# Kernel optimization log

Measured on AMD Instinct MI355X. Metric: run time of the kernel, lower is better.

## Reference

```python
import jax, jax.numpy as jnp
import numpy as np

N = 1024
BATCH = 256


def setup_inputs() -> dict:
    key = jax.random.key(0)
    k1, k2 = jax.random.split(key)
    log_alpha = jax.random.normal(k1, (BATCH, N), dtype=jnp.float32)
    W = jax.random.normal(k2, (N, N), dtype=jnp.float32)  # unnormalized transition matrix
    return {"log_alpha": log_alpha, "W": W}


def reference(log_alpha, W):
    # log_softmax over dim=0 (columns are distributions over next state)
    log_T = jax.nn.log_softmax(W, axis=0)  # [N, N]
    # log_domain_matmul: out[i, m] = logsumexp_j( log_T[i, j] + log_alpha[m, j] )
    # then transpose back -> out[m, i]
    # broadcast-add cube [BATCH, N, N] then logsumexp over j (tropical-semiring matmul)
    out = jax.scipy.special.logsumexp(
        log_T[None, :, :] + log_alpha[:, None, :], axis=2
    )  # [BATCH, N]
    return out
```

## Files before the change

### kernel.cpp

```cpp
#include <hip/hip_runtime.h>
#include <hip/hip_bf16.h>

#define N 1024
#define BATCH 256
#define LPAD 136

typedef __attribute__((ext_vector_type(4))) short short4v;
typedef __attribute__((ext_vector_type(8))) short short8;
typedef __attribute__((ext_vector_type(4))) float f32x4;

static __device__ __forceinline__ ushort bfbits(float f) {
    union { __hip_bfloat16 h; ushort u; } cv; cv.h = __float2bfloat16(f); return cv.u;
}
static __device__ __forceinline__ float bf2f(ushort u) {
    union { ushort u; __hip_bfloat16 h; } cv; cv.u = u; return __bfloat162float(cv.h);
}

__global__ __launch_bounds__(256) void k1_psplit(const float* __restrict__ W,
                                                 float* __restrict__ psum,
                                                 ushort* __restrict__ Ph,
                                                 ushort* __restrict__ Pl) {
    const int t = threadIdx.x, lane = t & 63, w = t >> 6;
    const int cg = blockIdx.x & 3, slab = blockIdx.x >> 2;
    const int c = cg * 256 + lane * 4;
    __shared__ f32x4 sm[4][64];
    f32x4 acc = {0.f, 0.f, 0.f, 0.f};
#pragma unroll
    for (int it = 0; it < 4; ++it) {
        const int row = slab * 16 + w * 4 + it;
        const f32x4 v = *(const f32x4*)(W + row * N + c);
        short4v ph, pl;
        f32x4 e;
#pragma unroll
        for (int x = 0; x < 4; ++x) {
            e[x] = __expf(v[x]);
            const ushort h = bfbits(e[x]);
            ph[x] = (short)h;
            pl[x] = (short)bfbits(e[x] - bf2f(h));
        }
        *(short4v*)(Ph + row * N + c) = ph;
        *(short4v*)(Pl + row * N + c) = pl;
        acc += e;
    }
    sm[w][lane] = acc;
    __syncthreads();
    if (t < 64)
        *(f32x4*)(psum + slab * N + c) =
            sm[0][lane] + sm[1][lane] + sm[2][lane] + sm[3][lane];
}

__global__ __launch_bounds__(256) void k2_qsplit(const float* __restrict__ la,
                                                 const float* __restrict__ psum,
                                                 ushort* __restrict__ Qh,
                                                 ushort* __restrict__ Ql) {
    const int t = threadIdx.x;
    const int cg = blockIdx.x & 7, mg = blockIdx.x >> 3;
    const int c0 = cg * 128;
    __shared__ f32x4 smred[8][32];
    __shared__ float lcs[128];

    const int q = t & 31, sg = t >> 5;
    f32x4 a = {0.f, 0.f, 0.f, 0.f};
#pragma unroll
    for (int i = 0; i < 8; ++i)
        a += *(const f32x4*)(psum + (sg * 8 + i) * N + c0 + q * 4);
    smred[sg][q] = a;
    __syncthreads();
    if (t < 32) {
        f32x4 s = {0.f, 0.f, 0.f, 0.f};
#pragma unroll
        for (int g = 0; g < 8; ++g) s += smred[g][t];
#pragma unroll
        for (int x = 0; x < 4; ++x) lcs[t * 4 + x] = __logf(s[x]);
    }
    __syncthreads();

    const int row = mg * 16 + (t >> 4);
    const int cc  = (t & 15) * 8;
    const float* pla = la + row * N + c0 + cc;
    const f32x4 v0 = *(const f32x4*)(pla);
    const f32x4 v1 = *(const f32x4*)(pla + 4);
    short8 qh, ql;
#pragma unroll
    for (int x = 0; x < 8; ++x) {
        const float lv = (x < 4) ? v0[x] : v1[x - 4];
        const float qv = __expf(lv - lcs[cc + x]);
        const ushort h = bfbits(qv);
        qh[x] = (short)h;
        ql[x] = (short)bfbits(qv - bf2f(h));
    }
    *(short8*)(Qh + row * N + c0 + cc) = qh;
    *(short8*)(Ql + row * N + c0 + cc) = ql;
}

__global__ __launch_bounds__(512) void k3_mm(const ushort* __restrict__ Qh,
                                             const ushort* __restrict__ Ql,
                                             const ushort* __restrict__ Ph,
                                             const ushort* __restrict__ Pl,
                                             float* __restrict__ out) {
    __shared__ ushort sQh[32 * LPAD], sQl[32 * LPAD];
    __shared__ ushort sPh[32 * LPAD], sPl[32 * LPAD];

    const int t    = threadIdx.x;
    const int lane = t & 63;
    const int wid  = t >> 6;
    const int wm   = (wid >> 1) & 1;
    const int wn   = wid & 1;
    const int g    = wid >> 2;
    const int m0   = (blockIdx.x >> 5) * 32;
    const int i0   = (blockIdx.x & 31) * 32;

    const int srow = t >> 4;
    const int skc  = (t & 15) * 8;
    const ushort* gQh = Qh + (m0 + srow) * N + skc;
    const ushort* gQl = Ql + (m0 + srow) * N + skc;
    const ushort* gPh = Ph + (i0 + srow) * N + skc;
    const ushort* gPl = Pl + (i0 + srow) * N + skc;
    const int sdst = srow * LPAD + skc;

    const int aoff = (wm * 16 + (lane & 15)) * LPAD + g * 64 + (lane >> 4) * 8;
    const int boff = (wn * 16 + (lane & 15)) * LPAD + g * 64 + (lane >> 4) * 8;

    f32x4 acc = {0.f, 0.f, 0.f, 0.f};

    short8 vqh = *(const short8*)(gQh);
    short8 vql = *(const short8*)(gQl);
    short8 vph = *(const short8*)(gPh);
    short8 vpl = *(const short8*)(gPl);

    for (int k0 = 0; k0 < N; k0 += 128) {
        __syncthreads();
        *(short8*)&sQh[sdst] = vqh;
        *(short8*)&sQl[sdst] = vql;
        *(short8*)&sPh[sdst] = vph;
        *(short8*)&sPl[sdst] = vpl;
        if (k0 + 128 < N) {
            vqh = *(const short8*)(gQh + k0 + 128);
            vql = *(const short8*)(gQl + k0 + 128);
            vph = *(const short8*)(gPh + k0 + 128);
            vpl = *(const short8*)(gPl + k0 + 128);
        }
        __syncthreads();
#pragma unroll
        for (int ks = 0; ks < 2; ++ks) {
            const short8 aQh = *(const short8*)&sQh[aoff + ks * 32];
            const short8 aQl = *(const short8*)&sQl[aoff + ks * 32];
            const short8 bPh = *(const short8*)&sPh[boff + ks * 32];
            const short8 bPl = *(const short8*)&sPl[boff + ks * 32];
            acc = __builtin_amdgcn_mfma_f32_16x16x32_bf16(aQh, bPh, acc, 0, 0, 0);
            acc = __builtin_amdgcn_mfma_f32_16x16x32_bf16(aQh, bPl, acc, 0, 0, 0);
            acc = __builtin_amdgcn_mfma_f32_16x16x32_bf16(aQl, bPh, acc, 0, 0, 0);
        }
    }

    __syncthreads();
    f32x4* red = (f32x4*)sQh;
    red[wid * 64 + lane] = acc;
    __syncthreads();
    if (wid < 4) {
        const f32x4 s = red[wid * 64 + lane] + red[(wid + 4) * 64 + lane];
        const int om = m0 + wm * 16 + (lane >> 4) * 4;
        const int oi = i0 + wn * 16 + (lane & 15);
#pragma unroll
        for (int r = 0; r < 4; ++r)
            out[(om + r) * N + oi] = __logf(s[r]);
    }
}

extern "C" void kernel_launch(void* const* d_in, const int* in_sizes, int n_in,
                              void* d_out, int out_size, void* d_ws, size_t ws_size,
                              hipStream_t stream) {
    const float* la = (const float*)d_in[0];
    const float* W  = (const float*)d_in[1];
    float* out = (float*)d_out;

    char* ws = (char*)d_ws;
    float*  psum = (float*)ws;
    ushort* Ph   = (ushort*)(ws + (256 << 10));
    ushort* Pl   = Ph + (size_t)N * N;
    ushort* Qh   = Pl + (size_t)N * N;
    ushort* Ql   = Qh + (size_t)BATCH * N;

    k1_psplit<<<256, 256, 0, stream>>>(W, psum, Ph, Pl);
    k2_qsplit<<<128, 256, 0, stream>>>(la, psum, Qh, Ql);
    k3_mm<<<256, 512, 0, stream>>>(Qh, Ql, Ph, Pl, out);
}
```

Before: 68.65 us.

## Load MFMA operands directly from global into registers, drop LDS staging

The matmul kernel no longer stages Q and P tiles through shared memory. Each wave loads its MFMA fragments straight from global memory into a register double buffer, prefetching the second half of its K range while computing the first, and splits the work across two accumulators to shorten the dependency chain. This removes the per-step LDS writes, reads and barriers, at the cost of more registers and global loads that are less coalesced. The Q-prep kernel is also regridded to twice as many blocks, each handling 64 columns, to spread that work across more CUs.

After: 78.50 us. 1.14x slower.

```diff
diff --git a/kernel.cpp b/kernel.cpp
--- a/kernel.cpp
+++ b/kernel.cpp
@@ -3,7 +3,6 @@
 
 #define N 1024
 #define BATCH 256
-#define LPAD 136
 
 typedef __attribute__((ext_vector_type(4))) short short4v;
 typedef __attribute__((ext_vector_type(8))) short short8;
@@ -54,43 +53,37 @@
                                                  ushort* __restrict__ Qh,
                                                  ushort* __restrict__ Ql) {
     const int t = threadIdx.x;
-    const int cg = blockIdx.x & 7, mg = blockIdx.x >> 3;
-    const int c0 = cg * 128;
-    __shared__ f32x4 smred[8][32];
-    __shared__ float lcs[128];
+    const int cg = blockIdx.x & 15, mg = blockIdx.x >> 4;
+    const int c0 = cg * 64;
+    __shared__ float smred[4][64];
+    __shared__ float lcs[64];
 
-    const int q = t & 31, sg = t >> 5;
-    f32x4 a = {0.f, 0.f, 0.f, 0.f};
+    {
+        const int col = t & 63, sg = t >> 6;
+        float a = 0.f;
 #pragma unroll
-    for (int i = 0; i < 8; ++i)
-        a += *(const f32x4*)(psum + (sg * 8 + i) * N + c0 + q * 4);
-    smred[sg][q] = a;
+        for (int i = 0; i < 16; ++i)
+            a += psum[(sg * 16 + i) * N + c0 + col];
+        smred[sg][col] = a;
+    }
     __syncthreads();
-    if (t < 32) {
-        f32x4 s = {0.f, 0.f, 0.f, 0.f};
-#pragma unroll
-        for (int g = 0; g < 8; ++g) s += smred[g][t];
-#pragma unroll
-        for (int x = 0; x < 4; ++x) lcs[t * 4 + x] = __logf(s[x]);
-    }
+    if (t < 64)
+        lcs[t] = __logf(smred[0][t] + smred[1][t] + smred[2][t] + smred[3][t]);
     __syncthreads();
 
     const int row = mg * 16 + (t >> 4);
-    const int cc  = (t & 15) * 8;
-    const float* pla = la + row * N + c0 + cc;
-    const f32x4 v0 = *(const f32x4*)(pla);
-    const f32x4 v1 = *(const f32x4*)(pla + 4);
-    short8 qh, ql;
+    const int cc  = (t & 15) * 4;
+    const f32x4 v = *(const f32x4*)(la + row * N + c0 + cc);
+    short4v qh, ql;
 #pragma unroll
-    for (int x = 0; x < 8; ++x) {
-        const float lv = (x < 4) ? v0[x] : v1[x - 4];
-        const float qv = __expf(lv - lcs[cc + x]);
+    for (int x = 0; x < 4; ++x) {
+        const float qv = __expf(v[x] - lcs[cc + x]);
         const ushort h = bfbits(qv);
         qh[x] = (short)h;
         ql[x] = (short)bfbits(qv - bf2f(h));
     }
-    *(short8*)(Qh + row * N + c0 + cc) = qh;
-    *(short8*)(Ql + row * N + c0 + cc) = ql;
+    *(short4v*)(Qh + row * N + c0 + cc) = qh;
+    *(short4v*)(Ql + row * N + c0 + cc) = ql;
 }
 
 __global__ __launch_bounds__(512) void k3_mm(const ushort* __restrict__ Qh,
@@ -98,8 +91,7 @@
                                              const ushort* __restrict__ Ph,
                                              const ushort* __restrict__ Pl,
                                              float* __restrict__ out) {
-    __shared__ ushort sQh[32 * LPAD], sQl[32 * LPAD];
-    __shared__ ushort sPh[32 * LPAD], sPl[32 * LPAD];
+    __shared__ f32x4 red[512];
 
     const int t    = threadIdx.x;
     const int lane = t & 63;
@@ -110,52 +102,46 @@
     const int m0   = (blockIdx.x >> 5) * 32;
     const int i0   = (blockIdx.x & 31) * 32;
 
-    const int srow = t >> 4;
-    const int skc  = (t & 15) * 8;
-    const ushort* gQh = Qh + (m0 + srow) * N + skc;
-    const ushort* gQl = Ql + (m0 + srow) * N + skc;
-    const ushort* gPh = Ph + (i0 + srow) * N + skc;
-    const ushort* gPl = Pl + (i0 + srow) * N + skc;
-    const int sdst = srow * LPAD + skc;
+    const int kb = g * 512 + (lane >> 4) * 8;
+    const ushort* pAh = Qh + (m0 + wm * 16 + (lane & 15)) * N + kb;
+    const ushort* pAl = Ql + (m0 + wm * 16 + (lane & 15)) * N + kb;
+    const ushort* pBh = Ph + (i0 + wn * 16 + (lane & 15)) * N + kb;
+    const ushort* pBl = Pl + (i0 + wn * 16 + (lane & 15)) * N + kb;
 
-    const int aoff = (wm * 16 + (lane & 15)) * LPAD + g * 64 + (lane >> 4) * 8;
-    const int boff = (wn * 16 + (lane & 15)) * LPAD + g * 64 + (lane >> 4) * 8;
+    short8 rAh[8], rAl[8], rBh[8], rBl[8];
+#pragma unroll
+    for (int c = 0; c < 8; ++c) {
+        rAh[c] = *(const short8*)(pAh + c * 32);
+        rAl[c] = *(const short8*)(pAl + c * 32);
+        rBh[c] = *(const short8*)(pBh + c * 32);
+        rBl[c] = *(const short8*)(pBl + c * 32);
+    }
 
-    f32x4 acc = {0.f, 0.f, 0.f, 0.f};
+    f32x4 acc0 = {0.f, 0.f, 0.f, 0.f};
+    f32x4 acc1 = {0.f, 0.f, 0.f, 0.f};
 
-    short8 vqh = *(const short8*)(gQh);
-    short8 vql = *(const short8*)(gQl);
-    short8 vph = *(const short8*)(gPh);
-    short8 vpl = *(const short8*)(gPl);
-
-    for (int k0 = 0; k0 < N; k0 += 128) {
-        __syncthreads();
-        *(short8*)&sQh[sdst] = vqh;
-        *(short8*)&sQl[sdst] = vql;
-        *(short8*)&sPh[sdst] = vph;
-        *(short8*)&sPl[sdst] = vpl;
-        if (k0 + 128 < N) {
-            vqh = *(const short8*)(gQh + k0 + 128);
-            vql = *(const short8*)(gQl + k0 + 128);
-            vph = *(const short8*)(gPh + k0 + 128);
-            vpl = *(const short8*)(gPl + k0 + 128);
+#pragma unroll
+    for (int ks = 0; ks < 16; ++ks) {
+        const int c = ks & 7;
+        const short8 ah = rAh[c], al = rAl[c], bh = rBh[c], bl = rBl[c];
+        if (ks < 8) {
+            rAh[c] = *(const short8*)(pAh + (ks + 8) * 32);
+            rAl[c] = *(const short8*)(pAl + (ks + 8) * 32);
+            rBh[c] = *(const short8*)(pBh + (ks + 8) * 32);
+            rBl[c] = *(const short8*)(pBl + (ks + 8) * 32);
         }
-        __syncthreads();
-#pragma unroll
-        for (int ks = 0; ks < 2; ++ks) {
-            const short8 aQh = *(const short8*)&sQh[aoff + ks * 32];
-            const short8 aQl = *(const short8*)&sQl[aoff + ks * 32];
-            const short8 bPh = *(const short8*)&sPh[boff + ks * 32];
-            const short8 bPl = *(const short8*)&sPl[boff + ks * 32];
-            acc = __builtin_amdgcn_mfma_f32_16x16x32_bf16(aQh, bPh, acc, 0, 0, 0);
-            acc = __builtin_amdgcn_mfma_f32_16x16x32_bf16(aQh, bPl, acc, 0, 0, 0);
-            acc = __builtin_amdgcn_mfma_f32_16x16x32_bf16(aQl, bPh, acc, 0, 0, 0);
+        if (ks & 1) {
+            acc1 = __builtin_amdgcn_mfma_f32_16x16x32_bf16(ah, bh, acc1, 0, 0, 0);
+            acc1 = __builtin_amdgcn_mfma_f32_16x16x32_bf16(ah, bl, acc1, 0, 0, 0);
+            acc1 = __builtin_amdgcn_mfma_f32_16x16x32_bf16(al, bh, acc1, 0, 0, 0);
+        } else {
+            acc0 = __builtin_amdgcn_mfma_f32_16x16x32_bf16(ah, bh, acc0, 0, 0, 0);
+            acc0 = __builtin_amdgcn_mfma_f32_16x16x32_bf16(ah, bl, acc0, 0, 0, 0);
+            acc0 = __builtin_amdgcn_mfma_f32_16x16x32_bf16(al, bh, acc0, 0, 0, 0);
         }
     }
 
-    __syncthreads();
-    f32x4* red = (f32x4*)sQh;
-    red[wid * 64 + lane] = acc;
+    red[wid * 64 + lane] = acc0 + acc1;
     __syncthreads();
     if (wid < 4) {
         const f32x4 s = red[wid * 64 + lane] + red[(wid + 4) * 64 + lane];
@@ -182,6 +168,6 @@
     ushort* Ql   = Qh + (size_t)BATCH * N;
 
     k1_psplit<<<256, 256, 0, stream>>>(W, psum, Ph, Pl);
-    k2_qsplit<<<128, 256, 0, stream>>>(la, psum, Qh, Ql);
+    k2_qsplit<<<256, 256, 0, stream>>>(la, psum, Qh, Ql);
     k3_mm<<<256, 512, 0, stream>>>(Qh, Ql, Ph, Pl, out);
 }
```
